# Optimization experiments

Measured on AMD Instinct MI355X. Metric: run time of the kernel, lower is better.

## Reference

```python
import jax, jax.numpy as jnp
import numpy as np

B, S, D, H = 2, 2048, 1024, 16
DH = D // H
LAMBDA_INIT = 0.8
EPS = 1e-5


def setup_inputs() -> dict:
    key = jax.random.key(0)
    ks = jax.random.split(key, 12)
    inp = {
        "inputs": jax.random.normal(ks[0], (B, S, D), jnp.float32),
        # projection weights stored as [in, out] for right-multiplication
        "wq0": jax.random.normal(ks[1], (D, H * DH), jnp.float32) * 0.02,
        "wq1": jax.random.normal(ks[2], (D, H * DH), jnp.float32) * 0.02,
        "wk0": jax.random.normal(ks[3], (D, H * DH), jnp.float32) * 0.02,
        "wk1": jax.random.normal(ks[4], (D, H * DH), jnp.float32) * 0.02,
        "wv": jax.random.normal(ks[5], (D, H * DH), jnp.float32) * 0.02,
        "wo": jax.random.normal(ks[6], (H * DH, D), jnp.float32) * 0.02,
        # lambda parameter vectors (scaled so exp(dot) stays sane)
        "l0": jax.random.normal(ks[7], (DH,), jnp.float32) * 0.1,
        "l1": jax.random.normal(ks[8], (DH,), jnp.float32) * 0.1,
        "l2": jax.random.normal(ks[9], (DH,), jnp.float32) * 0.1,
        "l3": jax.random.normal(ks[10], (DH,), jnp.float32) * 0.1,
        # per-head LayerNorm params stacked: [H, DH]
        "ln_w": jnp.ones((H, DH), jnp.float32),
        "ln_b": jnp.zeros((H, DH), jnp.float32),
    }
    return inp


def _forward(inputs, wq0, wq1, wk0, wk1, wv, wo, l0, l1, l2, l3, ln_w, ln_b):
    b, s, d = inputs.shape

    def proj(w):  # [b,s,d] @ [d,H*DH] -> [b,H,s,DH]
        return jnp.einsum("bsd,de->bse", inputs, w).reshape(b, s, H, DH).transpose(0, 2, 1, 3)

    q0, q1 = proj(wq0), proj(wq1)
    k0, k1 = proj(wk0), proj(wk1)
    v = proj(wv)

    scale = jax.lax.rsqrt(jnp.float32(DH))
    # ALiBi bias: slope_h * (pos_i - pos_j)
    slopes = (2.0 ** (-8.0 * jnp.arange(1, H + 1, dtype=jnp.float32) / H))  # [H]
    pos = jnp.arange(s, dtype=jnp.float32)
    pos_diff = pos[:, None] - pos[None, :]  # [s,s]
    bias = slopes[None, :, None, None] * pos_diff[None, None, :, :]  # [1,H,s,s]
    causal = jnp.where(jnp.triu(jnp.ones((s, s), bool), 1), -jnp.inf, 0.0)[None, None]

    s0 = jnp.einsum("bhqd,bhkd->bhqk", q0, k0) * scale - bias + causal
    s1 = jnp.einsum("bhqd,bhkd->bhqk", q1, k1) * scale - bias + causal
    w0 = jax.nn.softmax(s0, axis=-1)
    w1 = jax.nn.softmax(s1, axis=-1)

    lamb = (-jnp.exp(jnp.dot(l0, l1)) + LAMBDA_INIT) + (-jnp.exp(jnp.dot(l2, l3)) + LAMBDA_INIT)
    diff_weights = w0 - lamb * w1

    heads = jnp.einsum("bhqk,bhkd->bhqd", diff_weights, v).transpose(0, 2, 1, 3)  # [b,s,H,DH]
    # per-head LayerNorm over DH (biased variance, eps=1e-5)
    mu = jnp.mean(heads, axis=-1, keepdims=True)
    var = jnp.mean((heads - mu) ** 2, axis=-1, keepdims=True)
    normed = (heads - mu) * jax.lax.rsqrt(var + EPS) * ln_w[None, None] + ln_b[None, None]

    attention = normed.reshape(b, s, H * DH)
    return jnp.einsum("bse,ed->bsd", attention, wo)


def reference(inputs, wq0, wq1, wk0, wk1, wv, wo, l0, l1, l2, l3, ln_w, ln_b):
    return _forward(inputs, wq0, wq1, wk0, wk1, wv, wo, l0, l1, l2, l3, ln_w, ln_b)
```

## Files before the change

### kernel.cpp

```cpp
#include <hip/hip_runtime.h>
#include <hip/hip_bf16.h>
#include <math.h>

#define S_LEN   2048
#define NH      16
#define DHEAD   64
#define UMEG    1048576

typedef __attribute__((ext_vector_type(8))) short short8;
typedef __attribute__((ext_vector_type(4))) short short4v;
typedef __attribute__((ext_vector_type(4))) float f32x4;
typedef __attribute__((ext_vector_type(16))) float f32x16;
typedef __attribute__((ext_vector_type(4))) int int4v;

__device__ __forceinline__ f32x4 mfma16(short8 a, short8 b, f32x4 c) {
    return __builtin_amdgcn_mfma_f32_16x16x32_bf16(a, b, c, 0, 0, 0);
}
__device__ __forceinline__ f32x16 mfma32(short8 a, short8 b, f32x16 c) {
    return __builtin_amdgcn_mfma_f32_32x32x16_bf16(a, b, c, 0, 0, 0);
}

__device__ __forceinline__ unsigned short f2bf(float f) {
    unsigned u = __builtin_bit_cast(unsigned, f);
    u = (u + 0x7FFFu + ((u >> 16) & 1u)) >> 16;
    return (unsigned short)u;
}
__device__ __forceinline__ float bf2f(short s) {
    unsigned u = ((unsigned)(unsigned short)s) << 16;
    return __builtin_bit_cast(float, u);
}

__device__ __forceinline__ int cvtpk(float lo, float hi) {
    int w;
    asm("v_cvt_pk_bf16_f32 %0, %1, %2" : "=v"(w) : "v"(lo), "v"(hi));
    return w;
}
__device__ __forceinline__ void pl32swap(int& a, int& b) {
    asm("v_permlane32_swap_b32 %0, %1" : "+v"(a), "+v"(b));
}

#define GLL16(gp, lp) __builtin_amdgcn_global_load_lds( \
    (const __attribute__((address_space(1))) void*)(gp), \
    (__attribute__((address_space(3))) void*)(lp), 16, 0, 0)

__global__ __launch_bounds__(256)
void convert_x(const float* __restrict__ x, short* __restrict__ xb)
{
    const int idx = (blockIdx.x * 256 + threadIdx.x) * 4;
    typedef __attribute__((ext_vector_type(4))) float f4;
    f4 v = *(const f4*)&x[idx];
    short4v o;
    o[0] = (short)f2bf(v[0]); o[1] = (short)f2bf(v[1]);
    o[2] = (short)f2bf(v[2]); o[3] = (short)f2bf(v[3]);
    *(short4v*)&xb[idx] = o;
}

__global__ __launch_bounds__(256)
void transp_w(const float* __restrict__ w0, const float* __restrict__ w1,
              const float* __restrict__ w2, const float* __restrict__ w3,
              const float* __restrict__ w4, const float* __restrict__ w5,
              short* __restrict__ wt)
{
    __shared__ float t[64][65];
    const int z = blockIdx.z;
    const float* src = (z == 0) ? w0 : (z == 1) ? w1 : (z == 2) ? w2
                     : (z == 3) ? w3 : (z == 4) ? w4 : w5;
    const float scale = (z <= 1) ? 0.125f * 1.44269504f : 1.0f;
    short* dst = wt + (size_t)z * UMEG;
    const int n0 = blockIdx.x * 64, k0 = blockIdx.y * 64;
    const int tid = threadIdx.x;
    const int c = tid & 63, rb = tid >> 6;
#pragma unroll
    for (int rr = 0; rr < 16; ++rr) {
        const int r = rr * 4 + rb;
        t[r][c] = src[(size_t)(k0 + r) * 1024 + n0 + c];
    }
    __syncthreads();
#pragma unroll
    for (int rr = 0; rr < 16; ++rr) {
        const int n = rr * 4 + rb;
        dst[(size_t)(n0 + n) * 1024 + k0 + c] = (short)f2bf(t[c][n] * scale);
    }
}

__global__ __launch_bounds__(256)
void transp_v(const short* __restrict__ vsrc, short* __restrict__ vdst)
{
    __shared__ short t[64][68];
    const int bh = blockIdx.y;
    const int s0 = blockIdx.x * 64;
    const int tid = threadIdx.x;
    const int c = tid & 63, rb = tid >> 6;
    const size_t base = (size_t)bh * S_LEN * DHEAD;
#pragma unroll
    for (int rr = 0; rr < 16; ++rr) {
        const int r = rr * 4 + rb;
        t[r][c] = vsrc[base + (size_t)(s0 + r) * 64 + c];
    }
    __syncthreads();
#pragma unroll
    for (int rr = 0; rr < 16; ++rr) {
        const int d = rr * 4 + rb;
        vdst[base + (size_t)d * S_LEN + s0 + c] = t[c][d];
    }
}

__global__ __launch_bounds__(256)
void gemm128(const short* __restrict__ A, const short* __restrict__ Wt,
             short* __restrict__ outb, float* __restrict__ outf, int mode)
{
    __shared__ short As[128 * 64];
    __shared__ short Bs[128 * 64];
    const int tid = threadIdx.x;
    const int l = tid & 63, w = tid >> 6;
    const int wm = w >> 1, wn = w & 1;
    const int m0 = blockIdx.y * 128;
    const int n0 = blockIdx.x * 128;
    const short* Bt = Wt + (size_t)blockIdx.z * UMEG;
    const int srow = l >> 3;
    const int schunk = (l & 7) ^ srow;

    f32x4 acc[4][4];
#pragma unroll
    for (int i = 0; i < 4; ++i)
#pragma unroll
        for (int j = 0; j < 4; ++j)
            acc[i][j] = (f32x4){0.f, 0.f, 0.f, 0.f};

    for (int k0 = 0; k0 < 1024; k0 += 64) {
        __syncthreads();
#pragma unroll
        for (int ii = 0; ii < 4; ++ii) {
            const int i = w * 4 + ii;
            GLL16(A  + (size_t)(m0 + 8 * i + srow) * 1024 + k0 + schunk * 8, &As[i * 512]);
            GLL16(Bt + (size_t)(n0 + 8 * i + srow) * 1024 + k0 + schunk * 8, &Bs[i * 512]);
        }
        __syncthreads();
#pragma unroll
        for (int kh = 0; kh < 2; ++kh) {
            short8 af[4], bfr[4];
#pragma unroll
            for (int ft = 0; ft < 4; ++ft) {
                const int row = wm * 64 + ft * 16 + (l & 15);
                const int ch = (kh * 4 + (l >> 4)) ^ (row & 7);
                af[ft] = *(const short8*)&As[row * 64 + ch * 8];
            }
#pragma unroll
            for (int nt = 0; nt < 4; ++nt) {
                const int row = wn * 64 + nt * 16 + (l & 15);
                const int ch = (kh * 4 + (l >> 4)) ^ (row & 7);
                bfr[nt] = *(const short8*)&Bs[row * 64 + ch * 8];
            }
#pragma unroll
            for (int i = 0; i < 4; ++i)
#pragma unroll
                for (int j = 0; j < 4; ++j)
                    acc[i][j] = mfma16(af[i], bfr[j], acc[i][j]);
        }
    }

    const size_t zoff = (blockIdx.z == 4) ? (size_t)24 * UMEG
                                          : (size_t)blockIdx.z * (4 * UMEG);
#pragma unroll
    for (int i = 0; i < 4; ++i)
#pragma unroll
        for (int j = 0; j < 4; ++j)
#pragma unroll
            for (int r = 0; r < 4; ++r) {
                const int m = m0 + wm * 64 + i * 16 + (l >> 4) * 4 + r;
                const int n = n0 + wn * 64 + j * 16 + (l & 15);
                const float v = acc[i][j][r];
                if (mode == 0) {
                    const int b = m >> 11, s = m & 2047;
                    const int h = n >> 6, dh = n & 63;
                    outb[zoff + (((size_t)(b * NH + h)) * S_LEN + s) * DHEAD + dh]
                        = (short)f2bf(v);
                } else {
                    outf[(size_t)m * 1024 + n] = v;
                }
            }
}

__global__ __launch_bounds__(256, 2)
void diff_attn_mfma(const short* __restrict__ pbuf, const short* __restrict__ vtb,
                    short* __restrict__ partO, float* __restrict__ partml)
{
    __shared__ short Ks[2][3][64 * 64];

    const int tid = threadIdx.x;
    const int l = tid & 63, w = tid >> 6;
    const int il = l & 31, hi = l >> 5;
    const int bh = blockIdx.x;
    const int h = bh & 15;
    const int p = blockIdx.y >> 1;
    const int jh = blockIdx.y & 1;
    const int qtA = 15 - p, qtB = p;
    const int szA = qtA + 1, szB = qtB + 1;
    const int ktA0 = jh * szA, ktB0 = jh * szB;

    const size_t MAT = (size_t)4 * UMEG;
    const size_t hoff = (size_t)bh * S_LEN * DHEAD;
    const short* q0g = pbuf + 0 * MAT + hoff;
    const short* q1g = pbuf + 1 * MAT + hoff;
    const short* k0g = pbuf + 2 * MAT + hoff;
    const short* k1g = pbuf + 3 * MAT + hoff;
    const short* vtg = vtb + hoff;

    const float slope2 = exp2f(-0.5f * (float)(h + 1)) * 1.44269504f;

    int qt_cur = qtA;
    int rg = qtA * 128 + w * 32 + il;

    short8 qf0[4], qf1[4];
#pragma unroll
    for (int dblk = 0; dblk < 4; ++dblk) {
        qf0[dblk] = *(const short8*)&q0g[(size_t)rg * 64 + dblk * 16 + hi * 8];
        qf1[dblk] = *(const short8*)&q1g[(size_t)rg * 64 + dblk * 16 + hi * 8];
    }

    f32x16 ot0[2], ot1[2];
#pragma unroll
    for (int mb = 0; mb < 2; ++mb)
#pragma unroll
        for (int r = 0; r < 16; ++r) { ot0[mb][r] = 0.f; ot1[mb][r] = 0.f; }
    float m0r = -100000.f, m1r = -100000.f, l0r = 0.f, l1r = 0.f;

    const int srw = l >> 3;
    const int schunk = (l & 7) ^ srw;

#define KT_OF(s_) (((s_) < szA) ? (ktA0 + (s_)) : (ktB0 + ((s_) - szA)))

#define STAGE(kt_, bi_) do {                                                        \
    _Pragma("unroll")                                                               \
    for (int ii = 0; ii < 2; ++ii) {                                                \
        const int i_ = w * 2 + ii;                                                  \
        GLL16(k0g + (size_t)((kt_) * 64 + 8 * i_ + srw) * 64 + schunk * 8,          \
              &Ks[bi_][0][i_ * 512]);                                               \
        GLL16(k1g + (size_t)((kt_) * 64 + 8 * i_ + srw) * 64 + schunk * 8,          \
              &Ks[bi_][1][i_ * 512]);                                               \
        GLL16(vtg + (size_t)(8 * i_ + srw) * S_LEN + (kt_) * 64 + schunk * 8,       \
              &Ks[bi_][2][i_ * 512]);                                               \
    }                                                                               \
} while (0)

#define SAVEPART(qt_) do {                                                          \
    const int job_ = ((bh << 4) + (qt_)) * 2 + jh;                                  \
    if (hi == 0) {                                                                  \
        float4 mlv;                                                                 \
        mlv.x = m0r; mlv.y = l0r; mlv.z = m1r; mlv.w = l1r;                         \
        *(float4*)&partml[((size_t)job_ * 128 + w * 32 + il) * 4] = mlv;            \
    }                                                                               \
    _Pragma("unroll")                                                               \
    for (int mb_ = 0; mb_ < 2; ++mb_)                                               \
        _Pragma("unroll")                                                           \
        for (int rq_ = 0; rq_ < 4; ++rq_) {                                         \
            union { int wi[2]; short4v sv; } s0u, s1u;                              \
            s0u.wi[0] = cvtpk(ot0[mb_][rq_ * 4 + 0], ot0[mb_][rq_ * 4 + 1]);        \
            s0u.wi[1] = cvtpk(ot0[mb_][rq_ * 4 + 2], ot0[mb_][rq_ * 4 + 3]);        \
            s1u.wi[0] = cvtpk(ot1[mb_][rq_ * 4 + 0], ot1[mb_][rq_ * 4 + 1]);        \
            s1u.wi[1] = cvtpk(ot1[mb_][rq_ * 4 + 2], ot1[mb_][rq_ * 4 + 3]);        \
            const size_t ob_ = (size_t)job_ * 16384 + (size_t)mb_ * 4096            \
                               + rq_ * 1024 + hi * 512 + (w * 32 + il) * 4;         \
            *(short4v*)&partO[ob_] = s0u.sv;                                        \
            *(short4v*)&partO[ob_ + 8192] = s1u.sv;                                 \
        }                                                                           \
} while (0)

    STAGE(KT_OF(0), 0);

    for (int s = 0; s < 17; ++s) {
        const int cur = s & 1;
        if (s + 1 < 17) {
            const int ktn = KT_OF(s + 1);
            STAGE(ktn, cur ^ 1);
            asm volatile("s_waitcnt vmcnt(6)" ::: "memory");
        } else {
            asm volatile("s_waitcnt vmcnt(0)" ::: "memory");
        }
        __builtin_amdgcn_s_barrier();

        const int kt = KT_OF(s);
        const int qw0 = qt_cur * 128 + w * 32;
        if (kt * 64 <= qw0 + 31) {
            f32x16 s0[2], s1[2];
            const float cb0 = slope2 * (float)(kt * 64 + 4 * hi - rg) - m0r;
            const float dm = m0r - m1r;
#pragma unroll
            for (int kvb = 0; kvb < 2; ++kvb) {
                const float cb = cb0 + slope2 * (float)(kvb * 32);
#pragma unroll
                for (int r = 0; r < 16; ++r) {
                    const float pat = (float)((r & 3) + 8 * (r >> 2));
                    s0[kvb][r] = fmaf(slope2, pat, cb);
                    s1[kvb][r] = s0[kvb][r] + dm;
                }
            }

#pragma unroll
            for (int dblk = 0; dblk < 4; ++dblk)
#pragma unroll
                for (int kvb = 0; kvb < 2; ++kvb) {
                    const int rowA = kvb * 32 + il;
                    const int ch = (dblk * 2 + hi) ^ (rowA & 7);
                    const short8 k0f = *(const short8*)&Ks[cur][0][rowA * 64 + ch * 8];
                    const short8 k1f = *(const short8*)&Ks[cur][1][rowA * 64 + ch * 8];
                    s0[kvb] = mfma32(k0f, qf0[dblk], s0[kvb]);
                    s1[kvb] = mfma32(k1f, qf1[dblk], s1[kvb]);
                }

            if (kt * 64 + 63 > qw0) {
                const int mth = rg - kt * 64;
#pragma unroll
                for (int kvb = 0; kvb < 2; ++kvb)
#pragma unroll
                    for (int r = 0; r < 16; ++r) {
                        const int kvoff = kvb * 32 + (r & 3) + 8 * (r >> 2) + 4 * hi;
                        if (kvoff > mth) { s0[kvb][r] = -1e30f; s1[kvb][r] = -1e30f; }
                    }
            }

            float t0[8], t1[8];
#pragma unroll
            for (int r = 0; r < 8; ++r) {
                t0[r] = fmaxf(fmaxf(s0[0][r], s0[0][r + 8]), fmaxf(s0[1][r], s0[1][r + 8]));
                t1[r] = fmaxf(fmaxf(s1[0][r], s1[0][r + 8]), fmaxf(s1[1][r], s1[1][r + 8]));
            }
            float pm0 = fmaxf(fmaxf(fmaxf(t0[0], t0[1]), fmaxf(t0[2], t0[3])),
                              fmaxf(fmaxf(t0[4], t0[5]), fmaxf(t0[6], t0[7])));
            float pm1 = fmaxf(fmaxf(fmaxf(t1[0], t1[1]), fmaxf(t1[2], t1[3])),
                              fmaxf(fmaxf(t1[4], t1[5]), fmaxf(t1[6], t1[7])));
            pm0 = fmaxf(pm0, __shfl_xor(pm0, 32));
            pm1 = fmaxf(pm1, __shfl_xor(pm1, 32));

            if (__any(pm0 > 8.f || pm1 > 8.f)) {
                const float d0 = fmaxf(pm0, 0.f), d1 = fmaxf(pm1, 0.f);
                const float sc0 = __builtin_amdgcn_exp2f(-d0);
                const float sc1 = __builtin_amdgcn_exp2f(-d1);
#pragma unroll
                for (int mb = 0; mb < 2; ++mb)
#pragma unroll
                    for (int r = 0; r < 16; ++r) {
                        ot0[mb][r] *= sc0;
                        ot1[mb][r] *= sc1;
                    }
                l0r *= sc0; l1r *= sc1;
                m0r += d0; m1r += d1;
#pragma unroll
                for (int kvb = 0; kvb < 2; ++kvb)
#pragma unroll
                    for (int r = 0; r < 16; ++r) {
                        s0[kvb][r] -= d0;
                        s1[kvb][r] -= d1;
                    }
            }

#pragma unroll
            for (int kvb = 0; kvb < 2; ++kvb)
#pragma unroll
                for (int r = 0; r < 16; ++r) {
                    s0[kvb][r] = __builtin_amdgcn_exp2f(s0[kvb][r]);
                    s1[kvb][r] = __builtin_amdgcn_exp2f(s1[kvb][r]);
                }
            float u0[8], u1[8];
#pragma unroll
            for (int r = 0; r < 8; ++r) {
                u0[r] = (s0[0][r] + s0[0][r + 8]) + (s0[1][r] + s0[1][r + 8]);
                u1[r] = (s1[0][r] + s1[0][r + 8]) + (s1[1][r] + s1[1][r + 8]);
            }
            float rs0 = ((u0[0] + u0[1]) + (u0[2] + u0[3])) + ((u0[4] + u0[5]) + (u0[6] + u0[7]));
            float rs1 = ((u1[0] + u1[1]) + (u1[2] + u1[3])) + ((u1[4] + u1[5]) + (u1[6] + u1[7]));
            rs0 += __shfl_xor(rs0, 32);
            rs1 += __shfl_xor(rs1, 32);
            l0r += rs0; l1r += rs1;

            short8 pa0[4], pa1[4];
#pragma unroll
            for (int ks = 0; ks < 4; ++ks) {
                const int kvb = ks >> 1, rb = (ks & 1) * 8;
                int wa0 = cvtpk(s0[kvb][rb + 0], s0[kvb][rb + 1]);
                int wb0 = cvtpk(s0[kvb][rb + 2], s0[kvb][rb + 3]);
                int wc0 = cvtpk(s0[kvb][rb + 4], s0[kvb][rb + 5]);
                int wd0 = cvtpk(s0[kvb][rb + 6], s0[kvb][rb + 7]);
                pl32swap(wa0, wc0);
                pl32swap(wb0, wd0);
                int wa1 = cvtpk(s1[kvb][rb + 0], s1[kvb][rb + 1]);
                int wb1 = cvtpk(s1[kvb][rb + 2], s1[kvb][rb + 3]);
                int wc1 = cvtpk(s1[kvb][rb + 4], s1[kvb][rb + 5]);
                int wd1 = cvtpk(s1[kvb][rb + 6], s1[kvb][rb + 7]);
                pl32swap(wa1, wc1);
                pl32swap(wb1, wd1);
                union { int4v wi; short8 sv; } u0u, u1u;
                u0u.wi[0] = wa0; u0u.wi[1] = wb0; u0u.wi[2] = wc0; u0u.wi[3] = wd0;
                u1u.wi[0] = wa1; u1u.wi[1] = wb1; u1u.wi[2] = wc1; u1u.wi[3] = wd1;
                pa0[ks] = u0u.sv;
                pa1[ks] = u1u.sv;
            }

#pragma unroll
            for (int mb = 0; mb < 2; ++mb)
#pragma unroll
                for (int ks = 0; ks < 4; ++ks) {
                    const int rowV = mb * 32 + il;
                    const int ch = (ks * 2 + hi) ^ (rowV & 7);
                    const short8 vf = *(const short8*)&Ks[cur][2][rowV * 64 + ch * 8];
                    ot0[mb] = mfma32(vf, pa0[ks], ot0[mb]);
                    ot1[mb] = mfma32(vf, pa1[ks], ot1[mb]);
                }
        }
        __builtin_amdgcn_s_barrier();

        if (s == szA - 1) {
            SAVEPART(qtA);
#pragma unroll
            for (int mb = 0; mb < 2; ++mb)
#pragma unroll
                for (int r = 0; r < 16; ++r) { ot0[mb][r] = 0.f; ot1[mb][r] = 0.f; }
            m0r = -100000.f; m1r = -100000.f; l0r = 0.f; l1r = 0.f;
            qt_cur = qtB;
            rg = qtB * 128 + w * 32 + il;
#pragma unroll
            for (int dblk = 0; dblk < 4; ++dblk) {
                qf0[dblk] = *(const short8*)&q0g[(size_t)rg * 64 + dblk * 16 + hi * 8];
                qf1[dblk] = *(const short8*)&q1g[(size_t)rg * 64 + dblk * 16 + hi * 8];
            }
        }
    }
    SAVEPART(qtB);
#undef SAVEPART
#undef STAGE
#undef KT_OF
}

__global__ __launch_bounds__(256)
void merge_ln(const short* __restrict__ partO, const float* __restrict__ partml,
              const float* __restrict__ l0v, const float* __restrict__ l1v,
              const float* __restrict__ l2v, const float* __restrict__ l3v,
              const float* __restrict__ lnw, const float* __restrict__ lnb,
              short* __restrict__ atb)
{
    const int t = threadIdx.x;
    const int bh = blockIdx.y, b = bh >> 4, h = bh & 15;
    const int rl = t >> 2;
    const int srow = blockIdx.x * 64 + rl;
    const int qt = srow >> 7, rit = srow & 127;
    const int sub = t & 3, mb = sub >> 1, hs = sub & 1;

    float d01 = 0.f, d23 = 0.f;
    for (int i = 0; i < 64; ++i) { d01 += l0v[i] * l1v[i]; d23 += l2v[i] * l3v[i]; }
    const float lamb = (-__expf(d01) + 0.8f) + (-__expf(d23) + 0.8f);

    const size_t jA = ((size_t)(bh * 16 + qt)) * 2;
    const float4 mlA = *(const float4*)&partml[(jA * 128 + rit) * 4];
    const float4 mlB = *(const float4*)&partml[((jA + 1) * 128 + rit) * 4];
    const float mm0 = fmaxf(mlA.x, mlB.x);
    const float sA0 = exp2f(mlA.x - mm0), sB0 = exp2f(mlB.x - mm0);
    const float lc0 = mlA.y * sA0 + mlB.y * sB0;
    const float mm1 = fmaxf(mlA.z, mlB.z);
    const float sA1 = exp2f(mlA.z - mm1), sB1 = exp2f(mlB.z - mm1);
    const float lc1 = mlA.w * sA1 + mlB.w * sB1;
    const float i0 = 1.f / lc0, i1 = 1.f / lc1;

    float hv[16];
#pragma unroll
    for (int rq = 0; rq < 4; ++rq) {
        const size_t ob = jA * 16384 + (size_t)mb * 4096 + rq * 1024 + hs * 512 + rit * 4;
        const short4v a0 = *(const short4v*)&partO[ob];
        const short4v a1 = *(const short4v*)&partO[ob + 8192];
        const short4v b0 = *(const short4v*)&partO[ob + 16384];
        const short4v b1 = *(const short4v*)&partO[ob + 16384 + 8192];
#pragma unroll
        for (int j = 0; j < 4; ++j) {
            const float v0 = (bf2f(a0[j]) * sA0 + bf2f(b0[j]) * sB0) * i0;
            const float v1 = (bf2f(a1[j]) * sA1 + bf2f(b1[j]) * sB1) * i1;
            hv[rq * 4 + j] = v0 - lamb * v1;
        }
    }

    float s = 0.f;
#pragma unroll
    for (int r = 0; r < 16; ++r) s += hv[r];
    s += __shfl_xor(s, 1); s += __shfl_xor(s, 2);
    const float mu = s * (1.f / 64.f);
    float vs = 0.f;
#pragma unroll
    for (int r = 0; r < 16; ++r) { const float dd = hv[r] - mu; vs += dd * dd; }
    vs += __shfl_xor(vs, 1); vs += __shfl_xor(vs, 2);
    const float rstd = rsqrtf(vs * (1.f / 64.f) + 1e-5f);

    short* orow = atb + ((size_t)(b * S_LEN + srow)) * 1024 + h * 64;
#pragma unroll
    for (int rq = 0; rq < 4; ++rq) {
        const int d0 = mb * 32 + rq * 8 + hs * 4;
        float o[4];
#pragma unroll
        for (int j = 0; j < 4; ++j)
            o[j] = (hv[rq * 4 + j] - mu) * rstd * lnw[h * 64 + d0 + j] + lnb[h * 64 + d0 + j];
        union { int wi[2]; short4v sv; } st;
        st.wi[0] = cvtpk(o[0], o[1]);
        st.wi[1] = cvtpk(o[2], o[3]);
        *(short4v*)&orow[d0] = st.sv;
    }
}

extern "C" void kernel_launch(void* const* d_in, const int* in_sizes, int n_in,
                              void* d_out, int out_size, void* d_ws, size_t ws_size,
                              hipStream_t stream)
{
    (void)in_sizes; (void)n_in; (void)out_size; (void)ws_size;
    const float* x   = (const float*)d_in[0];
    const float* wq0 = (const float*)d_in[1];
    const float* wq1 = (const float*)d_in[2];
    const float* wk0 = (const float*)d_in[3];
    const float* wk1 = (const float*)d_in[4];
    const float* wv  = (const float*)d_in[5];
    const float* wo  = (const float*)d_in[6];
    const float* l0  = (const float*)d_in[7];
    const float* l1  = (const float*)d_in[8];
    const float* l2  = (const float*)d_in[9];
    const float* l3  = (const float*)d_in[10];
    const float* lnw = (const float*)d_in[11];
    const float* lnb = (const float*)d_in[12];
    float* out = (float*)d_out;
    short* ws = (short*)d_ws;

    short* wtcat  = ws;
    short* qk     = ws + (size_t)6  * UMEG;
    short* vtb    = ws + (size_t)22 * UMEG;
    short* atb    = ws + (size_t)26 * UMEG;
    short* xb     = atb;
    short* partO  = ws + (size_t)30 * UMEG;
    short* vorig  = partO;
    float* partml = (float*)(ws + (size_t)46 * UMEG);

    convert_x<<<4096, 256, 0, stream>>>(x, xb);
    transp_w<<<dim3(16, 16, 6), 256, 0, stream>>>(wq0, wq1, wk0, wk1, wv, wo, wtcat);
    gemm128<<<dim3(8, 32, 5), 256, 0, stream>>>(xb, wtcat, qk, nullptr, 0);
    transp_v<<<dim3(32, 32), 256, 0, stream>>>(vorig, vtb);
    diff_attn_mfma<<<dim3(32, 16), 256, 0, stream>>>(qk, vtb, partO, partml);
    merge_ln<<<dim3(32, 32), 256, 0, stream>>>(partO, partml,
                                               l0, l1, l2, l3, lnw, lnb, atb);
    gemm128<<<dim3(8, 32, 1), 256, 0, stream>>>(atb, wtcat + (size_t)5 * UMEG,
                                                nullptr, out, 1);
}
```

Baseline: 194.1 us.

## Double-buffer GEMM loads, triple-buffer attention K/V, add MFMA priority and XCD remap

The projection GEMM now double-buffers its A/B tiles in LDS, so the global-to-LDS loads for the next k-slice are issued before the MFMA work on the current one. Block indices are remapped so neighbouring tiles land on the same XCD, and occupancy is declared at two blocks per SM. The attention kernel moves from double to triple buffering of K/V tiles, which lets it drop the trailing barrier of each iteration. s_setprio raises wave priority around the MFMA loops in both kernels. The extra LDS use (double tiles in the GEMM, a third stage in attention) may lower occupancy, and the XCD remap assumes an 8x32 grid.

```diff
diff --git a/kernel.cpp b/kernel.cpp
--- a/kernel.cpp
+++ b/kernel.cpp
@@ -105,17 +105,19 @@
     }
 }
 
-__global__ __launch_bounds__(256)
+__global__ __launch_bounds__(256, 2)
 void gemm128(const short* __restrict__ A, const short* __restrict__ Wt,
              short* __restrict__ outb, float* __restrict__ outf, int mode)
 {
-    __shared__ short As[128 * 64];
-    __shared__ short Bs[128 * 64];
+    __shared__ short As[2][128 * 64];
+    __shared__ short Bs[2][128 * 64];
     const int tid = threadIdx.x;
     const int l = tid & 63, w = tid >> 6;
     const int wm = w >> 1, wn = w & 1;
-    const int m0 = blockIdx.y * 128;
-    const int n0 = blockIdx.x * 128;
+    const int lin = (int)blockIdx.x + 8 * (int)blockIdx.y;
+    const int xcd = lin & 7, j = lin >> 3;
+    const int m0 = (((xcd << 2) | (j >> 3))) * 128;
+    const int n0 = (j & 7) * 128;
     const short* Bt = Wt + (size_t)blockIdx.z * UMEG;
     const int srow = l >> 3;
     const int schunk = (l & 7) ^ srow;
@@ -124,18 +126,31 @@
 #pragma unroll
     for (int i = 0; i < 4; ++i)
 #pragma unroll
-        for (int j = 0; j < 4; ++j)
-            acc[i][j] = (f32x4){0.f, 0.f, 0.f, 0.f};
-
-    for (int k0 = 0; k0 < 1024; k0 += 64) {
-        __syncthreads();
-#pragma unroll
-        for (int ii = 0; ii < 4; ++ii) {
-            const int i = w * 4 + ii;
-            GLL16(A  + (size_t)(m0 + 8 * i + srow) * 1024 + k0 + schunk * 8, &As[i * 512]);
-            GLL16(Bt + (size_t)(n0 + 8 * i + srow) * 1024 + k0 + schunk * 8, &Bs[i * 512]);
+        for (int jj = 0; jj < 4; ++jj)
+            acc[i][jj] = (f32x4){0.f, 0.f, 0.f, 0.f};
+
+#define GSTAGE(t_, bi_) do {                                                        \
+    _Pragma("unroll")                                                               \
+    for (int ii = 0; ii < 4; ++ii) {                                                \
+        const int i_ = w * 4 + ii;                                                  \
+        GLL16(A  + (size_t)(m0 + 8 * i_ + srow) * 1024 + (t_) * 64 + schunk * 8,    \
+              &As[bi_][i_ * 512]);                                                  \
+        GLL16(Bt + (size_t)(n0 + 8 * i_ + srow) * 1024 + (t_) * 64 + schunk * 8,    \
+              &Bs[bi_][i_ * 512]);                                                  \
+    }                                                                               \
+} while (0)
+
+    GSTAGE(0, 0);
+
+    for (int t = 0; t < 16; ++t) {
+        const int cur = t & 1;
+        if (t + 1 < 16) {
+            GSTAGE(t + 1, cur ^ 1);
+            asm volatile("s_waitcnt vmcnt(8)" ::: "memory");
+        } else {
+            asm volatile("s_waitcnt vmcnt(0)" ::: "memory");
         }
-        __syncthreads();
+        __builtin_amdgcn_s_barrier();
 #pragma unroll
         for (int kh = 0; kh < 2; ++kh) {
             short8 af[4], bfr[4];
@@ -143,33 +158,37 @@
             for (int ft = 0; ft < 4; ++ft) {
                 const int row = wm * 64 + ft * 16 + (l & 15);
                 const int ch = (kh * 4 + (l >> 4)) ^ (row & 7);
-                af[ft] = *(const short8*)&As[row * 64 + ch * 8];
+                af[ft] = *(const short8*)&As[cur][row * 64 + ch * 8];
             }
 #pragma unroll
             for (int nt = 0; nt < 4; ++nt) {
                 const int row = wn * 64 + nt * 16 + (l & 15);
                 const int ch = (kh * 4 + (l >> 4)) ^ (row & 7);
-                bfr[nt] = *(const short8*)&Bs[row * 64 + ch * 8];
-            }
+                bfr[nt] = *(const short8*)&Bs[cur][row * 64 + ch * 8];
+            }
+            __builtin_amdgcn_s_setprio(1);
 #pragma unroll
             for (int i = 0; i < 4; ++i)
 #pragma unroll
-                for (int j = 0; j < 4; ++j)
-                    acc[i][j] = mfma16(af[i], bfr[j], acc[i][j]);
+                for (int jj = 0; jj < 4; ++jj)
+                    acc[i][jj] = mfma16(af[i], bfr[jj], acc[i][jj]);
+            __builtin_amdgcn_s_setprio(0);
         }
-    }
+        __builtin_amdgcn_s_barrier();
+    }
+#undef GSTAGE
 
     const size_t zoff = (blockIdx.z == 4) ? (size_t)24 * UMEG
                                           : (size_t)blockIdx.z * (4 * UMEG);
 #pragma unroll
     for (int i = 0; i < 4; ++i)
 #pragma unroll
-        for (int j = 0; j < 4; ++j)
+        for (int jj = 0; jj < 4; ++jj)
 #pragma unroll
             for (int r = 0; r < 4; ++r) {
                 const int m = m0 + wm * 64 + i * 16 + (l >> 4) * 4 + r;
-                const int n = n0 + wn * 64 + j * 16 + (l & 15);
-                const float v = acc[i][j][r];
+                const int n = n0 + wn * 64 + jj * 16 + (l & 15);
+                const float v = acc[i][jj][r];
                 if (mode == 0) {
                     const int b = m >> 11, s = m & 2047;
                     const int h = n >> 6, dh = n & 63;
@@ -185,7 +204,7 @@
 void diff_attn_mfma(const short* __restrict__ pbuf, const short* __restrict__ vtb,
                     short* __restrict__ partO, float* __restrict__ partml)
 {
-    __shared__ short Ks[2][3][64 * 64];
+    __shared__ short Ks[3][3][64 * 64];
 
     const int tid = threadIdx.x;
     const int l = tid & 63, w = tid >> 6;
@@ -269,16 +288,15 @@
     STAGE(KT_OF(0), 0);
 
     for (int s = 0; s < 17; ++s) {
-        const int cur = s & 1;
         if (s + 1 < 17) {
-            const int ktn = KT_OF(s + 1);
-            STAGE(ktn, cur ^ 1);
+            STAGE(KT_OF(s + 1), (s + 1) % 3);
             asm volatile("s_waitcnt vmcnt(6)" ::: "memory");
         } else {
             asm volatile("s_waitcnt vmcnt(0)" ::: "memory");
         }
         __builtin_amdgcn_s_barrier();
 
+        const int cur = s % 3;
         const int kt = KT_OF(s);
         const int qw0 = qt_cur * 128 + w * 32;
         if (kt * 64 <= qw0 + 31) {
@@ -296,6 +314,7 @@
                 }
             }
 
+            __builtin_amdgcn_s_setprio(1);
 #pragma unroll
             for (int dblk = 0; dblk < 4; ++dblk)
 #pragma unroll
@@ -307,6 +326,7 @@
                     s0[kvb] = mfma32(k0f, qf0[dblk], s0[kvb]);
                     s1[kvb] = mfma32(k1f, qf1[dblk], s1[kvb]);
                 }
+            __builtin_amdgcn_s_setprio(0);
 
             if (kt * 64 + 63 > qw0) {
                 const int mth = rg - kt * 64;
@@ -396,6 +416,7 @@
                 pa1[ks] = u1u.sv;
             }
 
+            __builtin_amdgcn_s_setprio(1);
 #pragma unroll
             for (int mb = 0; mb < 2; ++mb)
 #pragma unroll
@@ -406,8 +427,8 @@
                     ot0[mb] = mfma32(vf, pa0[ks], ot0[mb]);
                     ot1[mb] = mfma32(vf, pa1[ks], ot1[mb]);
                 }
+            __builtin_amdgcn_s_setprio(0);
         }
-        __builtin_amdgcn_s_barrier();
 
         if (s == szA - 1) {
             SAVEPART(qtA);
@@ -469,10 +490,10 @@
         const short4v b0 = *(const short4v*)&partO[ob + 16384];
         const short4v b1 = *(const short4v*)&partO[ob + 16384 + 8192];
 #pragma unroll
-        for (int j = 0; j < 4; ++j) {
-            const float v0 = (bf2f(a0[j]) * sA0 + bf2f(b0[j]) * sB0) * i0;
-            const float v1 = (bf2f(a1[j]) * sA1 + bf2f(b1[j]) * sB1) * i1;
-            hv[rq * 4 + j] = v0 - lamb * v1;
+        for (int jx = 0; jx < 4; ++jx) {
+            const float v0 = (bf2f(a0[jx]) * sA0 + bf2f(b0[jx]) * sB0) * i0;
+            const float v1 = (bf2f(a1[jx]) * sA1 + bf2f(b1[jx]) * sB1) * i1;
+            hv[rq * 4 + jx] = v0 - lamb * v1;
         }
     }
 
@@ -493,8 +514,8 @@
         const int d0 = mb * 32 + rq * 8 + hs * 4;
         float o[4];
 #pragma unroll
-        for (int j = 0; j < 4; ++j)
-            o[j] = (hv[rq * 4 + j] - mu) * rstd * lnw[h * 64 + d0 + j] + lnb[h * 64 + d0 + j];
+        for (int jx = 0; jx < 4; ++jx)
+            o[jx] = (hv[rq * 4 + jx] - mu) * rstd * lnw[h * 64 + d0 + jx] + lnb[h * 64 + d0 + jx];
         union { int wi[2]; short4v sv; } st;
         st.wi[0] = cvtpk(o[0], o[1]);
         st.wi[1] = cvtpk(o[2], o[3]);
```

Measured after the change: 179.8 us. -7.3%, faster.
